# Kernel tuning notes

Hardware: AMD Instinct MI355X
Metric: run time of the kernel (lower is better)

## Reference

```python
import jax, jax.numpy as jnp
import numpy as np

D_K = 64
SCALE = D_K ** (-0.5)
B, H, S = 2, 16, 2048


def setup_inputs() -> dict:
    key = jax.random.key(0)
    kq, kk, kv = jax.random.split(key, 3)
    q = jax.random.normal(kq, (B, H, S, D_K), dtype=jnp.float32)
    k = jax.random.normal(kk, (B, H, S, D_K), dtype=jnp.float32)
    v = jax.random.normal(kv, (B, H, S, D_K), dtype=jnp.float32)
    # causal mask: True means masked (matches torch masked_fill semantics)
    mask = jnp.triu(jnp.ones((S, S), dtype=bool), k=1)[None, None]  # [1,1,S,S]
    return {"q": q, "k": k, "v": v, "mask": mask}


def reference(q, k, v, mask) -> jnp.ndarray:
    # scores = q @ k^T  -> [B,H,S,S]
    scores = jnp.einsum("bhqd,bhkd->bhqk", q, k)
    # masked_fill(mask, -inf), then scale (as written in the source),
    # then softmax over the key axis. -inf * scale stays -inf.
    scores = jnp.where(mask, -jnp.inf, scores)
    attn = jax.nn.softmax(SCALE * scores, axis=-1)
    return jnp.einsum("bhqk,bhkd->bhqd", attn, v)
```

## Files before the change

### kernel.cpp

```cpp
#include <hip/hip_runtime.h>
#include <hip/hip_bf16.h>
#include <math.h>


constexpr int S  = 2048;
constexpr int D  = 64;
constexpr int BH = 32;
constexpr float SCALE = 0.125f;
constexpr float LOG2E = 1.4426950408889634f;
constexpr float QPRE  = SCALE * LOG2E;
constexpr int PSTR = 72;

typedef __attribute__((ext_vector_type(8))) short bf16x8;
typedef __attribute__((ext_vector_type(4))) short bf16x4;
typedef __attribute__((ext_vector_type(4))) float f32x4;

#if __has_builtin(__builtin_amdgcn_exp2f)
#define EXP2F(x) __builtin_amdgcn_exp2f(x)
#else
#define EXP2F(x) exp2f(x)
#endif

__device__ __forceinline__ short f2bf(float x) {
    union { __hip_bfloat16 b; short s; } u; u.b = __float2bfloat16(x); return u.s;
}

__device__ __forceinline__ void gload_lds16(const void* g, void* lds) {
    __builtin_amdgcn_global_load_lds(
        (const __attribute__((address_space(1))) unsigned int*)g,
        (__attribute__((address_space(3))) unsigned int*)lds, 16, 0, 0);
}

__global__ __launch_bounds__(256) void preconv_25993142075924(
    const float* __restrict__ Kg, const float* __restrict__ Vg,
    short* __restrict__ Kb, short* __restrict__ VT)
{
    const int kt = blockIdx.x, bh = blockIdx.y, tid = threadIdx.x;
    __shared__ float lt[64 * 65];
    const float* kp = Kg + (size_t)bh * S * D;
    const float* vp = Vg + (size_t)bh * S * D;
    short* kb = Kb + (size_t)bh * S * D;
    short* vt = VT + (size_t)bh * D * S;
    #pragma unroll
    for (int e = 0; e < 4; ++e) {
        int idx = (tid + e * 256) * 4;
        int r = idx >> 6, c = idx & 63;
        f32x4 k4 = *(const f32x4*)(kp + (size_t)(kt * 64 + r) * D + c);
        bf16x4 kb4;
        kb4[0] = f2bf(k4[0]); kb4[1] = f2bf(k4[1]);
        kb4[2] = f2bf(k4[2]); kb4[3] = f2bf(k4[3]);
        *(bf16x4*)(kb + (size_t)(kt * 64 + r) * D + c) = kb4;
        f32x4 v4 = *(const f32x4*)(vp + (size_t)(kt * 64 + r) * D + c);
        lt[(c + 0) * 65 + r] = v4[0];
        lt[(c + 1) * 65 + r] = v4[1];
        lt[(c + 2) * 65 + r] = v4[2];
        lt[(c + 3) * 65 + r] = v4[3];
    }
    __syncthreads();
    #pragma unroll
    for (int e = 0; e < 2; ++e) {
        int tt = tid + e * 256;
        int d  = tt >> 3;
        int j0 = (tt & 7) * 8;
        bf16x8 o;
        #pragma unroll
        for (int jj = 0; jj < 8; ++jj)
            o[jj] = f2bf(lt[d * 65 + j0 + jj]);
        *(bf16x8*)(vt + (size_t)d * S + kt * 64 + j0) = o;
    }
}

__global__ __launch_bounds__(256, 3) void attn_fwd_v7_25993142075924(
    const float* __restrict__ Qg, const short* __restrict__ Kb,
    const short* __restrict__ VT, float* __restrict__ Og)
{
    const int bh  = blockIdx.x;
    const int p   = 15 - (int)blockIdx.y;
    const int tid = threadIdx.x;
    const int wv  = tid >> 6;
    const int ln  = tid & 63;
    const int c16 = ln & 15;
    const int qd  = ln >> 4;

    const int qb  = 2 * p + (wv >> 1);
    const int q0  = qb * 64 + (wv & 1) * 32;
    const int nkt = 2 * p + 2;

    __shared__ __align__(16) short lk[2][64 * 64];
    __shared__ __align__(16) short lv[2][64 * 64];
    __shared__ __align__(16) short lp[4 * 16 * PSTR];
    short* lpw = lp + wv * 16 * PSTR;

    const float* qp = Qg + (size_t)bh * S * D;
    const short* kp = Kb + (size_t)bh * S * D;
    const short* vp = VT + (size_t)bh * D * S;
    float*       op = Og + (size_t)bh * S * D;

    const int srow0 = wv * 16 + (ln >> 3);
    const int sgrp0 = (ln & 7) ^ (srow0 & 7);
    const int srow1 = srow0 + 8;
    const int sgrp1 = (ln & 7) ^ (srow1 & 7);

    bf16x8 qf[2][2];
    #pragma unroll
    for (int qg = 0; qg < 2; ++qg) {
        const float* src = qp + (size_t)(q0 + qg * 16 + c16) * D + qd * 8;
        #pragma unroll
        for (int khf = 0; khf < 2; ++khf) {
            f32x4 a = *(const f32x4*)(src + khf * 32);
            f32x4 b = *(const f32x4*)(src + khf * 32 + 4);
            bf16x8 f;
            f[0] = f2bf(a[0] * QPRE); f[1] = f2bf(a[1] * QPRE);
            f[2] = f2bf(a[2] * QPRE); f[3] = f2bf(a[3] * QPRE);
            f[4] = f2bf(b[0] * QPRE); f[5] = f2bf(b[1] * QPRE);
            f[6] = f2bf(b[2] * QPRE); f[7] = f2bf(b[3] * QPRE);
            qf[qg][khf] = f;
        }
    }

    f32x4 oacc[2][4] = {{{0,0,0,0},{0,0,0,0},{0,0,0,0},{0,0,0,0}},
                        {{0,0,0,0},{0,0,0,0},{0,0,0,0},{0,0,0,0}}};
    float lpart[2][4] = {{0,0,0,0},{0,0,0,0}};

    gload_lds16(kp + (size_t)srow0 * D + sgrp0 * 8, &lk[0][(wv * 16 + 0) * 64]);
    gload_lds16(vp + (size_t)srow0 * S + sgrp0 * 8, &lv[0][(wv * 16 + 0) * 64]);
    gload_lds16(kp + (size_t)srow1 * D + sgrp1 * 8, &lk[0][(wv * 16 + 8) * 64]);
    gload_lds16(vp + (size_t)srow1 * S + sgrp1 * 8, &lv[0][(wv * 16 + 8) * 64]);
    __syncthreads();

    for (int kt = 0; kt < nkt; ++kt) {
        const int cur = kt & 1;
        if (kt + 1 < nkt) {
            const int nxt = cur ^ 1;
            const size_t kb0 = (size_t)(kt + 1) * 64;
            gload_lds16(kp + (kb0 + srow0) * D + sgrp0 * 8, &lk[nxt][(wv * 16 + 0) * 64]);
            gload_lds16(vp + (size_t)srow0 * S + kb0 + sgrp0 * 8, &lv[nxt][(wv * 16 + 0) * 64]);
            gload_lds16(kp + (kb0 + srow1) * D + sgrp1 * 8, &lk[nxt][(wv * 16 + 8) * 64]);
            gload_lds16(vp + (size_t)srow1 * S + kb0 + sgrp1 * 8, &lv[nxt][(wv * 16 + 8) * 64]);
        }

        if (kt <= qb) {
            bf16x8 kf[4][2], vf[4][2];
            #pragma unroll
            for (int nt = 0; nt < 4; ++nt) {
                const int row = nt * 16 + c16;
                #pragma unroll
                for (int khf = 0; khf < 2; ++khf) {
                    const int g = (khf * 4 + qd) ^ (row & 7);
                    kf[nt][khf] = *(const bf16x8*)&lk[cur][row * 64 + g * 8];
                    vf[nt][khf] = *(const bf16x8*)&lv[cur][row * 64 + g * 8];
                }
            }

            #pragma unroll
            for (int qg = 0; qg < 2; ++qg) {
                float t[4][4];
                #pragma unroll
                for (int nt = 0; nt < 4; ++nt) {
                    f32x4 acc = {0,0,0,0};
                    acc = __builtin_amdgcn_mfma_f32_16x16x32_bf16(qf[qg][0], kf[nt][0], acc, 0, 0, 0);
                    acc = __builtin_amdgcn_mfma_f32_16x16x32_bf16(qf[qg][1], kf[nt][1], acc, 0, 0, 0);
                    t[nt][0] = acc[0]; t[nt][1] = acc[1]; t[nt][2] = acc[2]; t[nt][3] = acc[3];
                }

                if (kt == qb) {
                    #pragma unroll
                    for (int nt = 0; nt < 4; ++nt) {
                        int j = kt * 64 + nt * 16 + c16;
                        #pragma unroll
                        for (int r = 0; r < 4; ++r)
                            if (j > q0 + qg * 16 + qd * 4 + r) t[nt][r] = -INFINITY;
                    }
                }

                float pval[4][4];
                #pragma unroll
                for (int nt = 0; nt < 4; ++nt)
                    #pragma unroll
                    for (int r = 0; r < 4; ++r) {
                        float pv = EXP2F(t[nt][r]);
                        pval[nt][r] = pv;
                        lpart[qg][r] += pv;
                    }

                #pragma unroll
                for (int nt = 0; nt < 4; ++nt)
                    #pragma unroll
                    for (int r = 0; r < 4; ++r)
                        lpw[(qd * 4 + r) * PSTR + nt * 16 + c16] = f2bf(pval[nt][r]);
                bf16x8 pf[2];
                #pragma unroll
                for (int khf = 0; khf < 2; ++khf)
                    pf[khf] = *(const bf16x8*)&lpw[c16 * PSTR + khf * 32 + qd * 8];

                #pragma unroll
                for (int dt = 0; dt < 4; ++dt) {
                    oacc[qg][dt] = __builtin_amdgcn_mfma_f32_16x16x32_bf16(pf[0], vf[dt][0], oacc[qg][dt], 0, 0, 0);
                    oacc[qg][dt] = __builtin_amdgcn_mfma_f32_16x16x32_bf16(pf[1], vf[dt][1], oacc[qg][dt], 0, 0, 0);
                }
            }
        }

        __syncthreads();
    }

    #pragma unroll
    for (int qg = 0; qg < 2; ++qg)
        #pragma unroll
        for (int r = 0; r < 4; ++r) {
            float s = lpart[qg][r];
            s += __shfl_xor(s, 1);
            s += __shfl_xor(s, 2);
            s += __shfl_xor(s, 4);
            s += __shfl_xor(s, 8);
            float inv = 1.0f / s;
            float* dst = op + (size_t)(q0 + qg * 16 + qd * 4 + r) * D;
            #pragma unroll
            for (int dt = 0; dt < 4; ++dt)
                dst[dt * 16 + c16] = oacc[qg][dt][r] * inv;
        }
}

__global__ __launch_bounds__(256) void attn_fwd_v1_25993142075924(
    const float* __restrict__ Qg, const float* __restrict__ Kg,
    const float* __restrict__ Vg, float* __restrict__ Og)
{
    constexpr int KSTR = 72;
    constexpr int BQ = 64, BK = 64;
    const int qt  = blockIdx.x;
    const int bh  = blockIdx.y;
    const int tid = threadIdx.x;
    const int wv  = tid >> 6;
    const int ln  = tid & 63;
    const int c16 = ln & 15;
    const int qd  = ln >> 4;

    __shared__ __align__(16) __hip_bfloat16 lk [BK][KSTR];
    __shared__ __align__(16) __hip_bfloat16 lvt[D ][KSTR];
    __shared__ __align__(16) __hip_bfloat16 lp [4][16][KSTR];

    const size_t hoff = (size_t)bh * S * D;
    const float* qp = Qg + hoff;
    const float* kp = Kg + hoff;
    const float* vp = Vg + hoff;
    float*       op = Og + hoff;
    const int q0 = qt * BQ;

    bf16x8 qf[2];
    {
        const float* src = qp + (size_t)(q0 + wv*16 + c16) * D + qd*8;
        #pragma unroll
        for (int kh = 0; kh < 2; ++kh) {
            f32x4 a = *(const f32x4*)(src + kh*32);
            f32x4 b = *(const f32x4*)(src + kh*32 + 4);
            bf16x8 f;
            f[0]=f2bf(a[0]*QPRE); f[1]=f2bf(a[1]*QPRE); f[2]=f2bf(a[2]*QPRE); f[3]=f2bf(a[3]*QPRE);
            f[4]=f2bf(b[0]*QPRE); f[5]=f2bf(b[1]*QPRE); f[6]=f2bf(b[2]*QPRE); f[7]=f2bf(b[3]*QPRE);
            qf[kh] = f;
        }
    }

    f32x4 oacc[4] = {{0,0,0,0},{0,0,0,0},{0,0,0,0},{0,0,0,0}};
    float mrun[4] = {-INFINITY,-INFINITY,-INFINITY,-INFINITY};
    float lrun[4] = {0.f,0.f,0.f,0.f};

    const int nkt = qt + 1;
    for (int kt = 0; kt < nkt; ++kt) {
        __syncthreads();
        #pragma unroll
        for (int e = 0; e < 4; ++e) {
            int idx = (tid + e*256) * 4;
            int row = idx >> 6, col = idx & 63;
            f32x4 k4 = *(const f32x4*)(kp + (size_t)(kt*BK + row)*D + col);
            bf16x4 kb;
            kb[0]=f2bf(k4[0]); kb[1]=f2bf(k4[1]); kb[2]=f2bf(k4[2]); kb[3]=f2bf(k4[3]);
            *(bf16x4*)&lk[row][col] = kb;
            f32x4 v4 = *(const f32x4*)(vp + (size_t)(kt*BK + row)*D + col);
            lvt[col+0][row] = __float2bfloat16(v4[0]);
            lvt[col+1][row] = __float2bfloat16(v4[1]);
            lvt[col+2][row] = __float2bfloat16(v4[2]);
            lvt[col+3][row] = __float2bfloat16(v4[3]);
        }
        __syncthreads();

        float t[4][4];
        #pragma unroll
        for (int nt = 0; nt < 4; ++nt) {
            f32x4 acc = {0,0,0,0};
            #pragma unroll
            for (int kh = 0; kh < 2; ++kh) {
                bf16x8 kf = *(const bf16x8*)&lk[nt*16 + c16][kh*32 + qd*8];
                acc = __builtin_amdgcn_mfma_f32_16x16x32_bf16(qf[kh], kf, acc, 0, 0, 0);
            }
            #pragma unroll
            for (int r = 0; r < 4; ++r) t[nt][r] = acc[r];
        }
        if (kt == nkt - 1) {
            #pragma unroll
            for (int nt = 0; nt < 4; ++nt) {
                int j = kt*BK + nt*16 + c16;
                #pragma unroll
                for (int r = 0; r < 4; ++r)
                    if (j > q0 + wv*16 + qd*4 + r) t[nt][r] = -INFINITY;
            }
        }

        float pval[4][4];
        #pragma unroll
        for (int r = 0; r < 4; ++r) {
            float tm = fmaxf(fmaxf(t[0][r], t[1][r]), fmaxf(t[2][r], t[3][r]));
            tm = fmaxf(tm, __shfl_xor(tm, 1));
            tm = fmaxf(tm, __shfl_xor(tm, 2));
            tm = fmaxf(tm, __shfl_xor(tm, 4));
            tm = fmaxf(tm, __shfl_xor(tm, 8));
            float mnew  = fmaxf(mrun[r], tm);
            float alpha = exp2f(mrun[r] - mnew);
            mrun[r] = mnew;
            float rs = 0.f;
            #pragma unroll
            for (int nt = 0; nt < 4; ++nt) {
                float pv = exp2f(t[nt][r] - mnew);
                pval[nt][r] = pv;
                rs += pv;
            }
            rs += __shfl_xor(rs, 1);
            rs += __shfl_xor(rs, 2);
            rs += __shfl_xor(rs, 4);
            rs += __shfl_xor(rs, 8);
            lrun[r] = lrun[r] * alpha + rs;
            #pragma unroll
            for (int dt = 0; dt < 4; ++dt) oacc[dt][r] *= alpha;
        }

        #pragma unroll
        for (int nt = 0; nt < 4; ++nt)
            #pragma unroll
            for (int r = 0; r < 4; ++r)
                lp[wv][qd*4 + r][nt*16 + c16] = __float2bfloat16(pval[nt][r]);
        bf16x8 pf[2];
        #pragma unroll
        for (int kh = 0; kh < 2; ++kh)
            pf[kh] = *(const bf16x8*)&lp[wv][c16][kh*32 + qd*8];

        #pragma unroll
        for (int dt = 0; dt < 4; ++dt) {
            #pragma unroll
            for (int kh = 0; kh < 2; ++kh) {
                bf16x8 vf = *(const bf16x8*)&lvt[dt*16 + c16][kh*32 + qd*8];
                oacc[dt] = __builtin_amdgcn_mfma_f32_16x16x32_bf16(pf[kh], vf, oacc[dt], 0, 0, 0);
            }
        }
    }

    #pragma unroll
    for (int r = 0; r < 4; ++r) {
        float inv = 1.0f / lrun[r];
        float* dst = op + (size_t)(q0 + wv*16 + qd*4 + r) * D;
        #pragma unroll
        for (int dt = 0; dt < 4; ++dt)
            dst[dt*16 + c16] = oacc[dt][r] * inv;
    }
}

extern "C" void kernel_launch(void* const* d_in, const int* in_sizes, int n_in,
                              void* d_out, int out_size, void* d_ws, size_t ws_size,
                              hipStream_t stream) {
    const float* q = (const float*)d_in[0];
    const float* k = (const float*)d_in[1];
    const float* v = (const float*)d_in[2];
    float* out = (float*)d_out;
    const size_t elems = (size_t)BH * S * D;
    const size_t need  = 2 * elems * sizeof(short);
    if (ws_size >= need) {
        short* Kb = (short*)d_ws;
        short* VT = Kb + elems;
        preconv_25993142075924<<<dim3(S / 64, BH), 256, 0, stream>>>(k, v, Kb, VT);
        attn_fwd_v7_25993142075924<<<dim3(BH, 16), 256, 0, stream>>>(q, Kb, VT, out);
    } else {
        attn_fwd_v1_25993142075924<<<dim3(S / 64, BH), 256, 0, stream>>>(q, k, v, out);
    }
}
```

Before: 142.0 us.

## Compute transposed S=K·Qᵀ so P stays in registers for PV MFMA

Swaps the MFMA operand order so scores come out transposed, with each lane holding one query column. The P fragments can then feed a 16x16x16 bf16 MFMA against V directly, removing the LDS round trip for P. The block shape also changes from 128 to 64 queries, with one 16-row query group per wave and twice as many blocks. This drops the skipped-tile waste, shrinks the row-sum reduction and allows vectorized output stores, at the cost of K/V tiles being loaded once per 64 queries instead of 128, which doubles K/V traffic.

```diff
diff --git a/kernel.cpp b/kernel.cpp
--- a/kernel.cpp
+++ b/kernel.cpp
@@ -14,6 +14,12 @@
 typedef __attribute__((ext_vector_type(8))) short bf16x8;
 typedef __attribute__((ext_vector_type(4))) short bf16x4;
 typedef __attribute__((ext_vector_type(4))) float f32x4;
+
+#if __has_builtin(__builtin_amdgcn_mfma_f32_16x16x16bf16_1k)
+#define HAS_MFMA_1K 1
+#else
+#define HAS_MFMA_1K 0
+#endif
 
 #if __has_builtin(__builtin_amdgcn_exp2f)
 #define EXP2F(x) __builtin_amdgcn_exp2f(x)
@@ -70,26 +76,27 @@
     }
 }
 
-__global__ __launch_bounds__(256, 3) void attn_fwd_v7_25993142075924(
+__global__ __launch_bounds__(256, 3) void attn_fwd_v8_25993142075924(
     const float* __restrict__ Qg, const short* __restrict__ Kb,
     const short* __restrict__ VT, float* __restrict__ Og)
 {
     const int bh  = blockIdx.x;
-    const int p   = 15 - (int)blockIdx.y;
+    const int qb  = 31 - (int)blockIdx.y;
     const int tid = threadIdx.x;
     const int wv  = tid >> 6;
     const int ln  = tid & 63;
     const int c16 = ln & 15;
     const int qd  = ln >> 4;
 
-    const int qb  = 2 * p + (wv >> 1);
-    const int q0  = qb * 64 + (wv & 1) * 32;
-    const int nkt = 2 * p + 2;
+    const int q0  = qb * 64 + wv * 16;
+    const int nkt = qb + 1;
 
     __shared__ __align__(16) short lk[2][64 * 64];
     __shared__ __align__(16) short lv[2][64 * 64];
+#if !HAS_MFMA_1K
     __shared__ __align__(16) short lp[4 * 16 * PSTR];
     short* lpw = lp + wv * 16 * PSTR;
+#endif
 
     const float* qp = Qg + (size_t)bh * S * D;
     const short* kp = Kb + (size_t)bh * S * D;
@@ -101,10 +108,9 @@
     const int srow1 = srow0 + 8;
     const int sgrp1 = (ln & 7) ^ (srow1 & 7);
 
-    bf16x8 qf[2][2];
-    #pragma unroll
-    for (int qg = 0; qg < 2; ++qg) {
-        const float* src = qp + (size_t)(q0 + qg * 16 + c16) * D + qd * 8;
+    bf16x8 qf[2];
+    {
+        const float* src = qp + (size_t)(q0 + c16) * D + qd * 8;
         #pragma unroll
         for (int khf = 0; khf < 2; ++khf) {
             f32x4 a = *(const f32x4*)(src + khf * 32);
@@ -114,13 +120,12 @@
             f[2] = f2bf(a[2] * QPRE); f[3] = f2bf(a[3] * QPRE);
             f[4] = f2bf(b[0] * QPRE); f[5] = f2bf(b[1] * QPRE);
             f[6] = f2bf(b[2] * QPRE); f[7] = f2bf(b[3] * QPRE);
-            qf[qg][khf] = f;
-        }
-    }
-
-    f32x4 oacc[2][4] = {{{0,0,0,0},{0,0,0,0},{0,0,0,0},{0,0,0,0}},
-                        {{0,0,0,0},{0,0,0,0},{0,0,0,0},{0,0,0,0}}};
-    float lpart[2][4] = {{0,0,0,0},{0,0,0,0}};
+            qf[khf] = f;
+        }
+    }
+
+    f32x4 oacc[4] = {{0,0,0,0},{0,0,0,0},{0,0,0,0},{0,0,0,0}};
+    float lsum = 0.f;
 
     gload_lds16(kp + (size_t)srow0 * D + sgrp0 * 8, &lk[0][(wv * 16 + 0) * 64]);
     gload_lds16(vp + (size_t)srow0 * S + sgrp0 * 8, &lv[0][(wv * 16 + 0) * 64]);
@@ -139,86 +144,103 @@
             gload_lds16(vp + (size_t)srow1 * S + kb0 + sgrp1 * 8, &lv[nxt][(wv * 16 + 8) * 64]);
         }
 
-        if (kt <= qb) {
-            bf16x8 kf[4][2], vf[4][2];
+#if HAS_MFMA_1K
+        bf16x4 vf[4][4];
+        #pragma unroll
+        for (int dt = 0; dt < 4; ++dt) {
+            const int row = dt * 16 + c16;
             #pragma unroll
             for (int nt = 0; nt < 4; ++nt) {
-                const int row = nt * 16 + c16;
+                const int gl = nt * 2 + (qd >> 1);
+                const int gp = gl ^ (c16 & 7);
+                vf[dt][nt] = *(const bf16x4*)&lv[cur][row * 64 + gp * 8 + (qd & 1) * 4];
+            }
+        }
+#endif
+
+        float t[4][4];
+        #pragma unroll
+        for (int nt = 0; nt < 4; ++nt) {
+            const int row = nt * 16 + c16;
+            f32x4 acc = {0,0,0,0};
+            #pragma unroll
+            for (int khf = 0; khf < 2; ++khf) {
+                const int g = (khf * 4 + qd) ^ (row & 7);
+                bf16x8 kf = *(const bf16x8*)&lk[cur][row * 64 + g * 8];
+                acc = __builtin_amdgcn_mfma_f32_16x16x32_bf16(kf, qf[khf], acc, 0, 0, 0);
+            }
+            t[nt][0] = acc[0]; t[nt][1] = acc[1]; t[nt][2] = acc[2]; t[nt][3] = acc[3];
+        }
+
+        if (kt == qb) {
+            #pragma unroll
+            for (int nt = 0; nt < 4; ++nt) {
                 #pragma unroll
-                for (int khf = 0; khf < 2; ++khf) {
-                    const int g = (khf * 4 + qd) ^ (row & 7);
-                    kf[nt][khf] = *(const bf16x8*)&lk[cur][row * 64 + g * 8];
-                    vf[nt][khf] = *(const bf16x8*)&lv[cur][row * 64 + g * 8];
+                for (int r = 0; r < 4; ++r) {
+                    int key = kt * 64 + nt * 16 + qd * 4 + r;
+                    if (key > q0 + c16) t[nt][r] = -INFINITY;
                 }
             }
-
-            #pragma unroll
-            for (int qg = 0; qg < 2; ++qg) {
-                float t[4][4];
-                #pragma unroll
-                for (int nt = 0; nt < 4; ++nt) {
-                    f32x4 acc = {0,0,0,0};
-                    acc = __builtin_amdgcn_mfma_f32_16x16x32_bf16(qf[qg][0], kf[nt][0], acc, 0, 0, 0);
-                    acc = __builtin_amdgcn_mfma_f32_16x16x32_bf16(qf[qg][1], kf[nt][1], acc, 0, 0, 0);
-                    t[nt][0] = acc[0]; t[nt][1] = acc[1]; t[nt][2] = acc[2]; t[nt][3] = acc[3];
-                }
-
-                if (kt == qb) {
-                    #pragma unroll
-                    for (int nt = 0; nt < 4; ++nt) {
-                        int j = kt * 64 + nt * 16 + c16;
-                        #pragma unroll
-                        for (int r = 0; r < 4; ++r)
-                            if (j > q0 + qg * 16 + qd * 4 + r) t[nt][r] = -INFINITY;
-                    }
-                }
-
-                float pval[4][4];
-                #pragma unroll
-                for (int nt = 0; nt < 4; ++nt)
-                    #pragma unroll
-                    for (int r = 0; r < 4; ++r) {
-                        float pv = EXP2F(t[nt][r]);
-                        pval[nt][r] = pv;
-                        lpart[qg][r] += pv;
-                    }
-
-                #pragma unroll
-                for (int nt = 0; nt < 4; ++nt)
-                    #pragma unroll
-                    for (int r = 0; r < 4; ++r)
-                        lpw[(qd * 4 + r) * PSTR + nt * 16 + c16] = f2bf(pval[nt][r]);
-                bf16x8 pf[2];
-                #pragma unroll
-                for (int khf = 0; khf < 2; ++khf)
-                    pf[khf] = *(const bf16x8*)&lpw[c16 * PSTR + khf * 32 + qd * 8];
-
-                #pragma unroll
-                for (int dt = 0; dt < 4; ++dt) {
-                    oacc[qg][dt] = __builtin_amdgcn_mfma_f32_16x16x32_bf16(pf[0], vf[dt][0], oacc[qg][dt], 0, 0, 0);
-                    oacc[qg][dt] = __builtin_amdgcn_mfma_f32_16x16x32_bf16(pf[1], vf[dt][1], oacc[qg][dt], 0, 0, 0);
-                }
-            }
-        }
+        }
+
+        float pval[4][4];
+        #pragma unroll
+        for (int nt = 0; nt < 4; ++nt)
+            #pragma unroll
+            for (int r = 0; r < 4; ++r) {
+                float pv = EXP2F(t[nt][r]);
+                pval[nt][r] = pv;
+                lsum += pv;
+            }
+
+#if HAS_MFMA_1K
+        #pragma unroll
+        for (int nt = 0; nt < 4; ++nt) {
+            bf16x4 pf;
+            pf[0] = f2bf(pval[nt][0]); pf[1] = f2bf(pval[nt][1]);
+            pf[2] = f2bf(pval[nt][2]); pf[3] = f2bf(pval[nt][3]);
+            #pragma unroll
+            for (int dt = 0; dt < 4; ++dt)
+                oacc[dt] = __builtin_amdgcn_mfma_f32_16x16x16bf16_1k(
+                    vf[dt][nt], pf, oacc[dt], 0, 0, 0);
+        }
+#else
+        #pragma unroll
+        for (int nt = 0; nt < 4; ++nt)
+            #pragma unroll
+            for (int r = 0; r < 4; ++r)
+                lpw[c16 * PSTR + nt * 16 + qd * 4 + r] = f2bf(pval[nt][r]);
+        bf16x8 pf2[2];
+        #pragma unroll
+        for (int khf = 0; khf < 2; ++khf)
+            pf2[khf] = *(const bf16x8*)&lpw[c16 * PSTR + khf * 32 + qd * 8];
+        #pragma unroll
+        for (int dt = 0; dt < 4; ++dt) {
+            const int row = dt * 16 + c16;
+            #pragma unroll
+            for (int khf = 0; khf < 2; ++khf) {
+                const int g = (khf * 4 + qd) ^ (row & 7);
+                bf16x8 vf8 = *(const bf16x8*)&lv[cur][row * 64 + g * 8];
+                oacc[dt] = __builtin_amdgcn_mfma_f32_16x16x32_bf16(vf8, pf2[khf], oacc[dt], 0, 0, 0);
+            }
+        }
+#endif
 
         __syncthreads();
     }
 
+    float s = lsum;
+    s += __shfl_xor(s, 16);
+    s += __shfl_xor(s, 32);
+    const float inv = 1.0f / s;
+    float* dst = op + (size_t)(q0 + c16) * D;
     #pragma unroll
-    for (int qg = 0; qg < 2; ++qg)
-        #pragma unroll
-        for (int r = 0; r < 4; ++r) {
-            float s = lpart[qg][r];
-            s += __shfl_xor(s, 1);
-            s += __shfl_xor(s, 2);
-            s += __shfl_xor(s, 4);
-            s += __shfl_xor(s, 8);
-            float inv = 1.0f / s;
-            float* dst = op + (size_t)(q0 + qg * 16 + qd * 4 + r) * D;
-            #pragma unroll
-            for (int dt = 0; dt < 4; ++dt)
-                dst[dt * 16 + c16] = oacc[qg][dt][r] * inv;
-        }
+    for (int dt = 0; dt < 4; ++dt) {
+        f32x4 o;
+        o[0] = oacc[dt][0] * inv; o[1] = oacc[dt][1] * inv;
+        o[2] = oacc[dt][2] * inv; o[3] = oacc[dt][3] * inv;
+        *(f32x4*)(dst + dt * 16 + qd * 4) = o;
+    }
 }
 
 __global__ __launch_bounds__(256) void attn_fwd_v1_25993142075924(
@@ -375,7 +397,7 @@
         short* Kb = (short*)d_ws;
         short* VT = Kb + elems;
         preconv_25993142075924<<<dim3(S / 64, BH), 256, 0, stream>>>(k, v, Kb, VT);
-        attn_fwd_v7_25993142075924<<<dim3(BH, 16), 256, 0, stream>>>(q, Kb, VT, out);
+        attn_fwd_v8_25993142075924<<<dim3(BH, 32), 256, 0, stream>>>(q, Kb, VT, out);
     } else {
         attn_fwd_v1_25993142075924<<<dim3(S / 64, BH), 256, 0, stream>>>(q, k, v, out);
     }
```

Result: faster. 135.7 us (-4.4%).
